# Kernel optimization log

Measured on AMD Instinct MI355X. Metric: run time of the kernel, lower is better.

Reference implementation:

```python
import jax, jax.numpy as jnp
import numpy as np

B, N, C, H, K = 4, 8192, 512, 8, 256
D = C // H  # head_dim = 64
EPS = 1e-6


def setup_inputs() -> dict:
    key = jax.random.key(0)
    k1, k2, k3 = jax.random.split(key, 3)
    x = jax.random.normal(k1, (B, N, C), dtype=jnp.float32)
    # Dense kernel (Keras default glorot-ish scale approximated; exact init irrelevant for math check)
    w_qkvv = jax.random.normal(k2, (C, 4 * C), dtype=jnp.float32) * (1.0 / np.sqrt(C))
    # UniformSqrtDim: uniform(-1/sqrt(K), 1/sqrt(K)) over shape (N, K)
    lim = 1.0 / np.sqrt(K)
    spatial_proj = jax.random.uniform(k3, (N, K), minval=-lim, maxval=lim, dtype=jnp.float32)
    temp_ca = jnp.ones((H, 1, 1), dtype=jnp.float32)
    temp_sa = jnp.ones((H, 1, 1), dtype=jnp.float32)
    return {"x": x, "w_qkvv": w_qkvv, "spatial_proj": spatial_proj,
            "temp_ca": temp_ca, "temp_sa": temp_sa}


def _safe_normalize(t):
    # normalize along last axis with clamped squared-sum (matches safe_normalize)
    sq = jnp.sum(t * t, axis=-1, keepdims=True)
    sq = jnp.where(sq < EPS, EPS, sq)
    return t / jnp.sqrt(sq)


def reference(x, w_qkvv, spatial_proj, temp_ca, temp_sa):
    b, n, c = x.shape
    qkvv = x @ w_qkvv  # [B, N, 4C]
    qkvv = qkvv.reshape(b, n, 4, H, D).transpose(2, 0, 3, 1, 4)  # [4, B, H, N, D]
    q, k, v_ca, v_sa = qkvv[0], qkvv[1], qkvv[2], qkvv[3]
    # transpose to [B, H, D, N]; normalize along N (tokens)
    q_t = q.transpose(0, 1, 3, 2)
    k_t = k.transpose(0, 1, 3, 2)
    v_ca_t = v_ca.transpose(0, 1, 3, 2)
    v_sa_t = v_sa.transpose(0, 1, 3, 2)
    q_norm = _safe_normalize(q_t)  # [B, H, D, N]
    k_norm = _safe_normalize(k_t)

    # --- Channel attention: [B,H,D,D] over small head_dim ---
    attn_ca = jnp.einsum('bhdn,bhen->bhde', q_norm, k_norm) * temp_ca
    attn_ca = jax.nn.softmax(attn_ca, axis=-1)
    x_ca = jnp.einsum('bhde,bhen->bhdn', attn_ca, v_ca_t)  # [B,H,D,N]
    x_ca = x_ca.transpose(0, 3, 1, 2).reshape(b, n, c)  # [B,N,C]

    # --- Spatial attention with N->K token projection ---
    k_proj = jnp.einsum('bhdn,nk->bhdk', k_norm, spatial_proj)  # [B,H,D,K]
    v_proj = jnp.einsum('bhdn,nk->bhdk', v_sa_t, spatial_proj)  # [B,H,D,K]
    attn_sa = jnp.einsum('bhdn,bhdk->bhnk', q_norm, k_proj) * temp_sa  # [B,H,N,K]
    attn_sa = jax.nn.softmax(attn_sa, axis=-1)
    x_sa = jnp.einsum('bhnk,bhdk->bhnd', attn_sa, v_proj)  # [B,H,N,D]
    x_sa = x_sa.transpose(0, 2, 1, 3).reshape(b, n, c)

    return x_ca + x_sa
```

## Files before the change

### kernel.cpp

```cpp
#include <hip/hip_runtime.h>
#include <hip/hip_bf16.h>

#define BATCH 4
#define SEQ   8192
#define CH    512
#define NHEAD 8
#define HDIM  64
#define KTOK  256
#define FOURC 2048

typedef __attribute__((ext_vector_type(8))) short bf16x8;
typedef __attribute__((ext_vector_type(4))) float f32x4;

#define GLOAD_LDS16(g, l)                                                      \
  __builtin_amdgcn_global_load_lds(                                            \
      (const __attribute__((address_space(1))) void*)(g),                      \
      (__attribute__((address_space(3))) void*)(l), 16, 0, 0)

__device__ __forceinline__ ushort bf16bits(float f) {
  __hip_bfloat16 b = __float2bfloat16(f);
  return *reinterpret_cast<ushort*>(&b);
}
__device__ __forceinline__ uint packbf2(float lo, float hi) {
  return (uint)bf16bits(lo) | ((uint)bf16bits(hi) << 16);
}

__global__ __launch_bounds__(256) void k_wt(
    const float* __restrict__ W, __hip_bfloat16* __restrict__ Wt) {
  __shared__ float tile[32][33];
  const int bx = blockIdx.x * 32;
  const int by = blockIdx.y * 32;
  const int t = threadIdx.x;
  const int r = t >> 5, c = t & 31;
#pragma unroll
  for (int it = 0; it < 4; ++it)
    tile[r + it * 8][c] = W[(size_t)(by + r + it * 8) * FOURC + bx + c];
  __syncthreads();
#pragma unroll
  for (int it = 0; it < 4; ++it) {
    int n = r + it * 8;
    Wt[(size_t)(bx + n) * CH + by + c] = __float2bfloat16(tile[c][n]);
  }
}

__global__ __launch_bounds__(256) void k_pt(
    const float* __restrict__ P, __hip_bfloat16* __restrict__ Pt) {
  __shared__ float tile[32][33];
  const int n0 = blockIdx.x * 32, k0 = blockIdx.y * 32;
  const int t = threadIdx.x, r = t >> 5, c = t & 31;
#pragma unroll
  for (int i = 0; i < 4; ++i)
    tile[r + i * 8][c] = P[(size_t)(n0 + r + i * 8) * KTOK + k0 + c];
  __syncthreads();
#pragma unroll
  for (int i = 0; i < 4; ++i)
    Pt[(size_t)(k0 + r + i * 8) * SEQ + n0 + c] = __float2bfloat16(tile[c][r + i * 8]);
}

__global__ __launch_bounds__(256) void k_xbf(
    const float* __restrict__ X, __hip_bfloat16* __restrict__ Xb) {
  size_t i = ((size_t)blockIdx.x * 256 + threadIdx.x) * 8;
  float4 a = *reinterpret_cast<const float4*>(&X[i]);
  float4 b = *reinterpret_cast<const float4*>(&X[i + 4]);
  ushort tmp[8];
  tmp[0] = bf16bits(a.x); tmp[1] = bf16bits(a.y);
  tmp[2] = bf16bits(a.z); tmp[3] = bf16bits(a.w);
  tmp[4] = bf16bits(b.x); tmp[5] = bf16bits(b.y);
  tmp[6] = bf16bits(b.z); tmp[7] = bf16bits(b.w);
  *reinterpret_cast<uint4*>(&Xb[i]) = *reinterpret_cast<const uint4*>(tmp);
}

__global__ __launch_bounds__(256) void k_gemm_mfma(
    const __hip_bfloat16* __restrict__ Xb, const __hip_bfloat16* __restrict__ Wt,
    __hip_bfloat16* __restrict__ QKVV) {
  __shared__ __align__(16) __hip_bfloat16 As[128 * 32];
  __shared__ __align__(16) __hip_bfloat16 Bs[128 * 32];
  const int t = threadIdx.x;
  const int wid = t >> 6, lane = t & 63;
  const int bid = blockIdx.x;
  const int xcd = bid & 7;
  const int l = bid >> 3;
  const int bm = (xcd * 32 + (l >> 4)) * 128;
  const int bn = (l & 15) * 128;
  const int wr = wid >> 1, wc = wid & 1;
  const int lrow = lane & 15, lk = (lane >> 4) * 8;
  const int srow = lane >> 2;
  const int sk8 = (lane & 3) * 8;
  f32x4 acc[4][4] = {};
  for (int k0 = 0; k0 < CH; k0 += 32) {
#pragma unroll
    for (int i = 0; i < 2; ++i) {
      const int c = wid * 2 + i;
      GLOAD_LDS16(&Xb[(size_t)(bm + c * 16 + srow) * CH + k0 + sk8], &As[c * 512]);
      GLOAD_LDS16(&Wt[(size_t)(bn + c * 16 + srow) * CH + k0 + sk8], &Bs[c * 512]);
    }
    __syncthreads();
    bf16x8 af[4], bfr[4];
#pragma unroll
    for (int i = 0; i < 4; ++i)
      af[i] = *reinterpret_cast<const bf16x8*>(&As[(wr * 64 + i * 16 + lrow) * 32 + lk]);
#pragma unroll
    for (int j = 0; j < 4; ++j)
      bfr[j] = *reinterpret_cast<const bf16x8*>(&Bs[(wc * 64 + j * 16 + lrow) * 32 + lk]);
#pragma unroll
    for (int i = 0; i < 4; ++i)
#pragma unroll
      for (int j = 0; j < 4; ++j)
        acc[i][j] = __builtin_amdgcn_mfma_f32_16x16x32_bf16(af[i], bfr[j], acc[i][j], 0, 0, 0);
    __syncthreads();
  }
  const int l4 = (lane >> 4) * 4;
#pragma unroll
  for (int i = 0; i < 4; ++i)
#pragma unroll
    for (int j = 0; j < 4; ++j) {
      int col = bn + wc * 64 + j * 16 + lrow;
#pragma unroll
      for (int r = 0; r < 4; ++r) {
        int row = bm + wr * 64 + i * 16 + l4 + r;
        QKVV[(size_t)row * FOURC + col] = __float2bfloat16(acc[i][j][r]);
      }
    }
}

__global__ __launch_bounds__(256) void k_finalize(
    const float* __restrict__ sumsq, float* __restrict__ invq, float* __restrict__ invk) {
  int i = blockIdx.x * 256 + threadIdx.x;
  if (i < 2048) {
    invq[i] = rsqrtf(fmaxf(sumsq[i], 1e-6f));
    invk[i] = rsqrtf(fmaxf(sumsq[2048 + i], 1e-6f));
  }
}

__global__ __launch_bounds__(256) void k_gram_stats(
    const __hip_bfloat16* __restrict__ QKVV, float* __restrict__ G,
    float* __restrict__ sumsq) {
  __shared__ __hip_bfloat16 qT[64][40];
  __shared__ __hip_bfloat16 kT[64][40];
  __shared__ float red[32][64];
  const int bh = blockIdx.y, b = bh >> 3, h = bh & 7;
  const int nbase = blockIdx.x * 512;
  const int t = threadIdx.x, w = t >> 6, lane = t & 63;
  const int l15 = lane & 15, g = lane >> 4;
  const int srow = t >> 3, sdq = (t & 7) * 8;
  f32x4 accg[4] = {};
  float sqq[8] = {}, sqk[8] = {};
  for (int n0 = nbase; n0 < nbase + 512; n0 += 32) {
    size_t gb = (size_t)(b * SEQ + n0 + srow) * FOURC + h * HDIM + sdq;
    uint4 uq = *reinterpret_cast<const uint4*>(&QKVV[gb]);
    uint4 uk = *reinterpret_cast<const uint4*>(&QKVV[gb + CH]);
    const __hip_bfloat16* hq = reinterpret_cast<const __hip_bfloat16*>(&uq);
    const __hip_bfloat16* hk = reinterpret_cast<const __hip_bfloat16*>(&uk);
#pragma unroll
    for (int j = 0; j < 8; ++j) {
      float fq = __bfloat162float(hq[j]);
      float fk = __bfloat162float(hk[j]);
      sqq[j] = fmaf(fq, fq, sqq[j]);
      sqk[j] = fmaf(fk, fk, sqk[j]);
      qT[sdq + j][srow] = hq[j];
      kT[sdq + j][srow] = hk[j];
    }
    __syncthreads();
    bf16x8 A[4];
#pragma unroll
    for (int dt = 0; dt < 4; ++dt)
      A[dt] = *reinterpret_cast<const bf16x8*>(&qT[dt * 16 + l15][g * 8]);
    bf16x8 B = *reinterpret_cast<const bf16x8*>(&kT[w * 16 + l15][g * 8]);
#pragma unroll
    for (int dt = 0; dt < 4; ++dt)
      accg[dt] = __builtin_amdgcn_mfma_f32_16x16x32_bf16(A[dt], B, accg[dt], 0, 0, 0);
    __syncthreads();
  }
#pragma unroll
  for (int j = 0; j < 8; ++j) red[srow][sdq + j] = sqq[j];
  __syncthreads();
  if (t < 64) {
    float tot = 0.f;
#pragma unroll
    for (int r = 0; r < 32; ++r) tot += red[r][t];
    atomicAdd(&sumsq[bh * 64 + t], tot);
  }
  __syncthreads();
#pragma unroll
  for (int j = 0; j < 8; ++j) red[srow][sdq + j] = sqk[j];
  __syncthreads();
  if (t < 64) {
    float tot = 0.f;
#pragma unroll
    for (int r = 0; r < 32; ++r) tot += red[r][t];
    atomicAdd(&sumsq[2048 + bh * 64 + t], tot);
  }
  float* gp = G + (size_t)bh * 4096;
#pragma unroll
  for (int dt = 0; dt < 4; ++dt)
#pragma unroll
    for (int r = 0; r < 4; ++r)
      atomicAdd(&gp[(dt * 16 + g * 4 + r) * 64 + w * 16 + l15], accg[dt][r]);
}

__global__ __launch_bounds__(64) void k_ca_softmax(
    float* __restrict__ G, const float* __restrict__ invq,
    const float* __restrict__ invk, const float* __restrict__ tca) {
  const int bh = blockIdx.x, h = bh & 7;
  const int d = threadIdx.x;
  float* row = G + (size_t)bh * 4096 + d * 64;
  const float s0 = invq[bh * 64 + d] * tca[h];
  float vals[64];
  float m = -3.0e38f;
#pragma unroll
  for (int e = 0; e < 64; ++e) {
    float v = row[e] * s0 * invk[bh * 64 + e];
    vals[e] = v;
    m = fmaxf(m, v);
  }
  float s = 0.f;
#pragma unroll
  for (int e = 0; e < 64; ++e) { vals[e] = __expf(vals[e] - m); s += vals[e]; }
  float r = 1.0f / s;
#pragma unroll
  for (int e = 0; e < 64; ++e) row[e] = vals[e] * r;
}

__global__ __launch_bounds__(256) void k_proj_mfma(
    const __hip_bfloat16* __restrict__ QKVV,
    const __hip_bfloat16* __restrict__ Pt,
    float* __restrict__ raw) {
  __shared__ __hip_bfloat16 cT[2][64][40];
  __shared__ __hip_bfloat16 pT[256][40];
  const int bh = blockIdx.y, b = bh >> 3, h = bh & 7;
  const int nbase = blockIdx.x * 1024;
  const int t = threadIdx.x, w = t >> 6, lane = t & 63;
  const int l15 = lane & 15, g = lane >> 4;
  const int comp = w >> 1, kh = w & 1;
  const int srow = t >> 3, sdq = (t & 7) * 8;
  f32x4 acc[4][8] = {};
  for (int n0 = nbase; n0 < nbase + 1024; n0 += 32) {
#pragma unroll
    for (int cc = 0; cc < 2; ++cc) {
      const int coff = cc ? 3 * CH : CH;
      uint4 u = *reinterpret_cast<const uint4*>(
          &QKVV[(size_t)(b * SEQ + n0 + srow) * FOURC + coff + h * HDIM + sdq]);
      const __hip_bfloat16* hp = reinterpret_cast<const __hip_bfloat16*>(&u);
#pragma unroll
      for (int j = 0; j < 8; ++j) cT[cc][sdq + j][srow] = hp[j];
    }
#pragma unroll
    for (int ps = 0; ps < 4; ++ps) {
      int k = ps * 64 + (t >> 2);
      int poff = (t & 3) * 8;
      *reinterpret_cast<uint4*>(&pT[k][poff]) =
          *reinterpret_cast<const uint4*>(&Pt[(size_t)k * SEQ + n0 + poff]);
    }
    __syncthreads();
    bf16x8 A[4], B[8];
#pragma unroll
    for (int dt = 0; dt < 4; ++dt)
      A[dt] = *reinterpret_cast<const bf16x8*>(&cT[comp][dt * 16 + l15][g * 8]);
#pragma unroll
    for (int kt = 0; kt < 8; ++kt)
      B[kt] = *reinterpret_cast<const bf16x8*>(&pT[(kh * 8 + kt) * 16 + l15][g * 8]);
#pragma unroll
    for (int dt = 0; dt < 4; ++dt)
#pragma unroll
      for (int kt = 0; kt < 8; ++kt)
        acc[dt][kt] = __builtin_amdgcn_mfma_f32_16x16x32_bf16(A[dt], B[kt], acc[dt][kt], 0, 0, 0);
    __syncthreads();
  }
  float* rp = raw + ((size_t)bh * 2 + comp) * (64 * 256);
#pragma unroll
  for (int dt = 0; dt < 4; ++dt)
#pragma unroll
    for (int kt = 0; kt < 8; ++kt)
#pragma unroll
      for (int r = 0; r < 4; ++r)
        atomicAdd(&rp[(dt * 16 + g * 4 + r) * 256 + (kh * 8 + kt) * 16 + l15],
                  acc[dt][kt][r]);
}

__global__ __launch_bounds__(256) void k_projfin(
    const float* __restrict__ raw, const float* __restrict__ invq,
    const float* __restrict__ invk, const float* __restrict__ tsa,
    __hip_bfloat16* __restrict__ kpT, __hip_bfloat16* __restrict__ vpT) {
  const int bh = blockIdx.x, h = bh & 7;
  const int t = threadIdx.x;
  __shared__ float tile[64][65];
  const float ts = tsa[h];
  const float* r0 = raw + (size_t)bh * 2 * 16384;
  for (int kc = 0; kc < 4; ++kc) {
    for (int i = t; i < 4096; i += 256) {
      int d = i >> 6, kk = i & 63;
      tile[d][kk] = r0[d * 256 + kc * 64 + kk];
    }
    __syncthreads();
    for (int i = t; i < 4096; i += 256) {
      int kk = i >> 6, d = i & 63;
      float sc = invq[bh * 64 + d] * invk[bh * 64 + d] * ts;
      kpT[(size_t)bh * 16384 + (kc * 64 + kk) * 64 + d] = __float2bfloat16(tile[d][kk] * sc);
    }
    __syncthreads();
  }
  const float* r1 = r0 + 16384;
  for (int i = t; i < 16384; i += 256)
    vpT[(size_t)bh * 16384 + i] = __float2bfloat16(r1[i]);
}

__global__ __launch_bounds__(256) void k_xout(
    const __hip_bfloat16* __restrict__ QKVV,
    const float* __restrict__ G,
    const __hip_bfloat16* __restrict__ kpT,
    const __hip_bfloat16* __restrict__ vpT,
    float* __restrict__ out) {
  __shared__ __hip_bfloat16 vs[64][264];
  __shared__ __hip_bfloat16 ps[4][16][264];
  __shared__ __hip_bfloat16 gs[64][72];
  const int bh = blockIdx.y, b = bh >> 3, h = bh & 7;
  const int nblk = blockIdx.x * 512;
  const int t = threadIdx.x, w = t >> 6, lane = t & 63;
  const int l15 = lane & 15, g = lane >> 4;
  for (int i = t; i < 2048; i += 256) {
    int d = i >> 5, k8 = (i & 31) * 8;
    *reinterpret_cast<uint4*>(&vs[d][k8]) =
        *reinterpret_cast<const uint4*>(&vpT[((size_t)bh * 64 + d) * 256 + k8]);
  }
  for (int i = t; i < 4096; i += 256)
    gs[i >> 6][i & 63] = __float2bfloat16(G[(size_t)bh * 4096 + i]);
  bf16x8 kA[2][16];
#pragma unroll
  for (int s = 0; s < 2; ++s)
#pragma unroll
    for (int f = 0; f < 16; ++f)
      kA[s][f] = *reinterpret_cast<const bf16x8*>(
          &kpT[((size_t)bh * 256 + f * 16 + l15) * 64 + s * 32 + g * 8]);
  __syncthreads();
  const __hip_bfloat16* qbase = QKVV + (size_t)b * SEQ * FOURC + h * HDIM;
  const __hip_bfloat16* vbase = qbase + 2 * CH;
  for (int c = w; c < 32; c += 4) {
    const int n0 = nblk + c * 16;
    bf16x8 qf[2], vf[2];
#pragma unroll
    for (int s = 0; s < 2; ++s) {
      qf[s] = *reinterpret_cast<const bf16x8*>(
          &qbase[(size_t)(n0 + l15) * FOURC + s * 32 + g * 8]);
      vf[s] = *reinterpret_cast<const bf16x8*>(
          &vbase[(size_t)(n0 + l15) * FOURC + s * 32 + g * 8]);
    }
    f32x4 o[4] = {};
#pragma unroll
    for (int dt = 0; dt < 4; ++dt) {
      bf16x8 g0 = *reinterpret_cast<const bf16x8*>(&gs[dt * 16 + l15][g * 8]);
      bf16x8 g1 = *reinterpret_cast<const bf16x8*>(&gs[dt * 16 + l15][32 + g * 8]);
      o[dt] = __builtin_amdgcn_mfma_f32_16x16x32_bf16(vf[0], g0, o[dt], 0, 0, 0);
      o[dt] = __builtin_amdgcn_mfma_f32_16x16x32_bf16(vf[1], g1, o[dt], 0, 0, 0);
    }
    f32x4 acc[16] = {};
#pragma unroll
    for (int f = 0; f < 16; ++f) {
      acc[f] = __builtin_amdgcn_mfma_f32_16x16x32_bf16(kA[0][f], qf[0], acc[f], 0, 0, 0);
      acc[f] = __builtin_amdgcn_mfma_f32_16x16x32_bf16(kA[1][f], qf[1], acc[f], 0, 0, 0);
    }
    float m = -3.0e38f;
#pragma unroll
    for (int f = 0; f < 16; ++f)
#pragma unroll
      for (int r = 0; r < 4; ++r) m = fmaxf(m, acc[f][r]);
    m = fmaxf(m, __shfl_xor(m, 16));
    m = fmaxf(m, __shfl_xor(m, 32));
    float sum = 0.f;
#pragma unroll
    for (int f = 0; f < 16; ++f)
#pragma unroll
      for (int r = 0; r < 4; ++r) {
        float e = __expf(acc[f][r] - m);
        acc[f][r] = e; sum += e;
      }
    sum += __shfl_xor(sum, 16);
    sum += __shfl_xor(sum, 32);
    const float rinv = 1.0f / sum;
#pragma unroll
    for (int f = 0; f < 16; ++f) {
      uint2 pw;
      pw.x = packbf2(acc[f][0] * rinv, acc[f][1] * rinv);
      pw.y = packbf2(acc[f][2] * rinv, acc[f][3] * rinv);
      *reinterpret_cast<uint2*>(&ps[w][l15][f * 16 + g * 4]) = pw;
    }
    __builtin_amdgcn_wave_barrier();
#pragma unroll
    for (int s = 0; s < 8; ++s) {
      bf16x8 pa = *reinterpret_cast<const bf16x8*>(&ps[w][l15][s * 32 + g * 8]);
#pragma unroll
      for (int dt = 0; dt < 4; ++dt) {
        bf16x8 vb = *reinterpret_cast<const bf16x8*>(&vs[dt * 16 + l15][s * 32 + g * 8]);
        o[dt] = __builtin_amdgcn_mfma_f32_16x16x32_bf16(pa, vb, o[dt], 0, 0, 0);
      }
    }
#pragma unroll
    for (int dt = 0; dt < 4; ++dt)
#pragma unroll
      for (int r = 0; r < 4; ++r) {
        size_t oo = ((size_t)(b * SEQ + n0 + g * 4 + r)) * CH + h * HDIM + dt * 16 + l15;
        out[oo] = o[dt][r];
      }
    __builtin_amdgcn_wave_barrier();
  }
}

extern "C" void kernel_launch(void* const* d_in, const int* in_sizes, int n_in,
                              void* d_out, int out_size, void* d_ws, size_t ws_size,
                              hipStream_t stream) {
  const float* x   = (const float*)d_in[0];
  const float* w   = (const float*)d_in[1];
  const float* sp  = (const float*)d_in[2];
  const float* tca = (const float*)d_in[3];
  const float* tsa = (const float*)d_in[4];
  float* out = (float*)d_out;
  char* ws = (char*)d_ws;

  __hip_bfloat16* qkvv = (__hip_bfloat16*)ws;
  __hip_bfloat16* wt   = (__hip_bfloat16*)(ws + 134217728);
  __hip_bfloat16* pt   = (__hip_bfloat16*)(ws + 136314880);
  __hip_bfloat16* xb   = (__hip_bfloat16*)(ws + 140509184);
  __hip_bfloat16* kpT  = (__hip_bfloat16*)(ws + 174063616);
  __hip_bfloat16* vpT  = (__hip_bfloat16*)(ws + 175112192);
  float* invq  = (float*)(ws + 176160768);
  float* invk  = (float*)(ws + 176168960);
  float* G     = (float*)(ws + 176177152);
  float* sumsq = (float*)(ws + 176701440);
  float* raw   = (float*)(ws + 176717824);

  hipMemsetAsync(G, 0, 524288 + 16384 + 4194304, stream);

  hipLaunchKernelGGL(k_wt, dim3(64, 16), dim3(256), 0, stream, w, wt);
  hipLaunchKernelGGL(k_pt, dim3(256, 8), dim3(256), 0, stream, sp, pt);
  hipLaunchKernelGGL(k_xbf, dim3(8192), dim3(256), 0, stream, x, xb);
  hipLaunchKernelGGL(k_gemm_mfma, dim3(4096), dim3(256), 0, stream, xb, wt, qkvv);
  hipLaunchKernelGGL(k_gram_stats, dim3(16, 32), dim3(256), 0, stream, qkvv, G, sumsq);
  hipLaunchKernelGGL(k_proj_mfma, dim3(8, 32), dim3(256), 0, stream, qkvv, pt, raw);
  hipLaunchKernelGGL(k_finalize, dim3(8), dim3(256), 0, stream, sumsq, invq, invk);
  hipLaunchKernelGGL(k_ca_softmax, dim3(32), dim3(64), 0, stream, G, invq, invk, tca);
  hipLaunchKernelGGL(k_projfin, dim3(32), dim3(256), 0, stream, raw, invq, invk, tsa, kpT, vpT);
  hipLaunchKernelGGL(k_xout, dim3(16, 32), dim3(256), 0, stream, qkvv, G, kpT, vpT, out);
}
```

Baseline: 310.4 us.

## Fuse Gram/stats with spatial projection and swizzle GEMM LDS layout

Merges the Q/K Gram-and-sum-of-squares kernel with the K/V spatial projection kernel, so the K tile is loaded from QKVV once per block and both reductions run in one pass with one fewer launch. The merged kernel uses the projection kernel's 1024-token chunks, which halves the block count of the Gram pass and raises register and LDS use per block. Separately, the GEMM's LDS write and read column indices are XOR-swizzled to reduce bank conflicts on the fragment loads. The swizzle must match exactly between the global_load_lds writes and the MFMA fragment reads, or results will be wrong.

```diff
diff --git a/kernel.cpp b/kernel.cpp
--- a/kernel.cpp
+++ b/kernel.cpp
@@ -83,9 +83,10 @@
   const int bm = (xcd * 32 + (l >> 4)) * 128;
   const int bn = (l & 15) * 128;
   const int wr = wid >> 1, wc = wid & 1;
-  const int lrow = lane & 15, lk = (lane >> 4) * 8;
+  const int lrow = lane & 15;
+  const int lk = (((lane >> 4) ^ ((lrow >> 1) & 3))) * 8;
   const int srow = lane >> 2;
-  const int sk8 = (lane & 3) * 8;
+  const int sk8 = (((lane & 3) ^ ((lane >> 3) & 3))) * 8;
   f32x4 acc[4][4] = {};
   for (int k0 = 0; k0 < CH; k0 += 32) {
 #pragma unroll
@@ -132,25 +133,32 @@
   }
 }
 
-__global__ __launch_bounds__(256) void k_gram_stats(
-    const __hip_bfloat16* __restrict__ QKVV, float* __restrict__ G,
-    float* __restrict__ sumsq) {
+__global__ __launch_bounds__(256) void k_qkstats(
+    const __hip_bfloat16* __restrict__ QKVV,
+    const __hip_bfloat16* __restrict__ Pt,
+    float* __restrict__ G, float* __restrict__ sumsq, float* __restrict__ raw) {
   __shared__ __hip_bfloat16 qT[64][40];
   __shared__ __hip_bfloat16 kT[64][40];
+  __shared__ __hip_bfloat16 vT[64][40];
+  __shared__ __hip_bfloat16 pT[256][40];
   __shared__ float red[32][64];
   const int bh = blockIdx.y, b = bh >> 3, h = bh & 7;
-  const int nbase = blockIdx.x * 512;
+  const int nbase = blockIdx.x * 1024;
   const int t = threadIdx.x, w = t >> 6, lane = t & 63;
   const int l15 = lane & 15, g = lane >> 4;
+  const int comp = w >> 1, kh = w & 1;
   const int srow = t >> 3, sdq = (t & 7) * 8;
+  f32x4 acc[4][8] = {};
   f32x4 accg[4] = {};
   float sqq[8] = {}, sqk[8] = {};
-  for (int n0 = nbase; n0 < nbase + 512; n0 += 32) {
+  for (int n0 = nbase; n0 < nbase + 1024; n0 += 32) {
     size_t gb = (size_t)(b * SEQ + n0 + srow) * FOURC + h * HDIM + sdq;
     uint4 uq = *reinterpret_cast<const uint4*>(&QKVV[gb]);
     uint4 uk = *reinterpret_cast<const uint4*>(&QKVV[gb + CH]);
+    uint4 uv = *reinterpret_cast<const uint4*>(&QKVV[gb + 3 * CH]);
     const __hip_bfloat16* hq = reinterpret_cast<const __hip_bfloat16*>(&uq);
     const __hip_bfloat16* hk = reinterpret_cast<const __hip_bfloat16*>(&uk);
+    const __hip_bfloat16* hv = reinterpret_cast<const __hip_bfloat16*>(&uv);
 #pragma unroll
     for (int j = 0; j < 8; ++j) {
       float fq = __bfloat162float(hq[j]);
@@ -159,16 +167,41 @@
       sqk[j] = fmaf(fk, fk, sqk[j]);
       qT[sdq + j][srow] = hq[j];
       kT[sdq + j][srow] = hk[j];
-    }
-    __syncthreads();
-    bf16x8 A[4];
-#pragma unroll
-    for (int dt = 0; dt < 4; ++dt)
-      A[dt] = *reinterpret_cast<const bf16x8*>(&qT[dt * 16 + l15][g * 8]);
-    bf16x8 B = *reinterpret_cast<const bf16x8*>(&kT[w * 16 + l15][g * 8]);
-#pragma unroll
-    for (int dt = 0; dt < 4; ++dt)
-      accg[dt] = __builtin_amdgcn_mfma_f32_16x16x32_bf16(A[dt], B, accg[dt], 0, 0, 0);
+      vT[sdq + j][srow] = hv[j];
+    }
+#pragma unroll
+    for (int ps = 0; ps < 4; ++ps) {
+      int k = ps * 64 + (t >> 2);
+      int poff = (t & 3) * 8;
+      *reinterpret_cast<uint4*>(&pT[k][poff]) =
+          *reinterpret_cast<const uint4*>(&Pt[(size_t)k * SEQ + n0 + poff]);
+    }
+    __syncthreads();
+    {
+      bf16x8 Aq[4];
+#pragma unroll
+      for (int dt = 0; dt < 4; ++dt)
+        Aq[dt] = *reinterpret_cast<const bf16x8*>(&qT[dt * 16 + l15][g * 8]);
+      bf16x8 Bk = *reinterpret_cast<const bf16x8*>(&kT[w * 16 + l15][g * 8]);
+#pragma unroll
+      for (int dt = 0; dt < 4; ++dt)
+        accg[dt] = __builtin_amdgcn_mfma_f32_16x16x32_bf16(Aq[dt], Bk, accg[dt], 0, 0, 0);
+    }
+    {
+      bf16x8 A[4], B[8];
+#pragma unroll
+      for (int dt = 0; dt < 4; ++dt)
+        A[dt] = comp ? *reinterpret_cast<const bf16x8*>(&vT[dt * 16 + l15][g * 8])
+                     : *reinterpret_cast<const bf16x8*>(&kT[dt * 16 + l15][g * 8]);
+#pragma unroll
+      for (int kt = 0; kt < 8; ++kt)
+        B[kt] = *reinterpret_cast<const bf16x8*>(&pT[(kh * 8 + kt) * 16 + l15][g * 8]);
+#pragma unroll
+      for (int dt = 0; dt < 4; ++dt)
+#pragma unroll
+        for (int kt = 0; kt < 8; ++kt)
+          acc[dt][kt] = __builtin_amdgcn_mfma_f32_16x16x32_bf16(A[dt], B[kt], acc[dt][kt], 0, 0, 0);
+    }
     __syncthreads();
   }
 #pragma unroll
@@ -196,6 +229,15 @@
 #pragma unroll
     for (int r = 0; r < 4; ++r)
       atomicAdd(&gp[(dt * 16 + g * 4 + r) * 64 + w * 16 + l15], accg[dt][r]);
+  float* rp = raw + ((size_t)bh * 2 + comp) * (64 * 256);
+#pragma unroll
+  for (int dt = 0; dt < 4; ++dt)
+#pragma unroll
+    for (int kt = 0; kt < 8; ++kt)
+#pragma unroll
+      for (int r = 0; r < 4; ++r)
+        atomicAdd(&rp[(dt * 16 + g * 4 + r) * 256 + (kh * 8 + kt) * 16 + l15],
+                  acc[dt][kt][r]);
 }
 
 __global__ __launch_bounds__(64) void k_ca_softmax(
@@ -219,62 +261,6 @@
   float r = 1.0f / s;
 #pragma unroll
   for (int e = 0; e < 64; ++e) row[e] = vals[e] * r;
-}
-
-__global__ __launch_bounds__(256) void k_proj_mfma(
-    const __hip_bfloat16* __restrict__ QKVV,
-    const __hip_bfloat16* __restrict__ Pt,
-    float* __restrict__ raw) {
-  __shared__ __hip_bfloat16 cT[2][64][40];
-  __shared__ __hip_bfloat16 pT[256][40];
-  const int bh = blockIdx.y, b = bh >> 3, h = bh & 7;
-  const int nbase = blockIdx.x * 1024;
-  const int t = threadIdx.x, w = t >> 6, lane = t & 63;
-  const int l15 = lane & 15, g = lane >> 4;
-  const int comp = w >> 1, kh = w & 1;
-  const int srow = t >> 3, sdq = (t & 7) * 8;
-  f32x4 acc[4][8] = {};
-  for (int n0 = nbase; n0 < nbase + 1024; n0 += 32) {
-#pragma unroll
-    for (int cc = 0; cc < 2; ++cc) {
-      const int coff = cc ? 3 * CH : CH;
-      uint4 u = *reinterpret_cast<const uint4*>(
-          &QKVV[(size_t)(b * SEQ + n0 + srow) * FOURC + coff + h * HDIM + sdq]);
-      const __hip_bfloat16* hp = reinterpret_cast<const __hip_bfloat16*>(&u);
-#pragma unroll
-      for (int j = 0; j < 8; ++j) cT[cc][sdq + j][srow] = hp[j];
-    }
-#pragma unroll
-    for (int ps = 0; ps < 4; ++ps) {
-      int k = ps * 64 + (t >> 2);
-      int poff = (t & 3) * 8;
-      *reinterpret_cast<uint4*>(&pT[k][poff]) =
-          *reinterpret_cast<const uint4*>(&Pt[(size_t)k * SEQ + n0 + poff]);
-    }
-    __syncthreads();
-    bf16x8 A[4], B[8];
-#pragma unroll
-    for (int dt = 0; dt < 4; ++dt)
-      A[dt] = *reinterpret_cast<const bf16x8*>(&cT[comp][dt * 16 + l15][g * 8]);
-#pragma unroll
-    for (int kt = 0; kt < 8; ++kt)
-      B[kt] = *reinterpret_cast<const bf16x8*>(&pT[(kh * 8 + kt) * 16 + l15][g * 8]);
-#pragma unroll
-    for (int dt = 0; dt < 4; ++dt)
-#pragma unroll
-      for (int kt = 0; kt < 8; ++kt)
-        acc[dt][kt] = __builtin_amdgcn_mfma_f32_16x16x32_bf16(A[dt], B[kt], acc[dt][kt], 0, 0, 0);
-    __syncthreads();
-  }
-  float* rp = raw + ((size_t)bh * 2 + comp) * (64 * 256);
-#pragma unroll
-  for (int dt = 0; dt < 4; ++dt)
-#pragma unroll
-    for (int kt = 0; kt < 8; ++kt)
-#pragma unroll
-      for (int r = 0; r < 4; ++r)
-        atomicAdd(&rp[(dt * 16 + g * 4 + r) * 256 + (kh * 8 + kt) * 16 + l15],
-                  acc[dt][kt][r]);
 }
 
 __global__ __launch_bounds__(256) void k_projfin(
@@ -433,8 +419,7 @@
   hipLaunchKernelGGL(k_pt, dim3(256, 8), dim3(256), 0, stream, sp, pt);
   hipLaunchKernelGGL(k_xbf, dim3(8192), dim3(256), 0, stream, x, xb);
   hipLaunchKernelGGL(k_gemm_mfma, dim3(4096), dim3(256), 0, stream, xb, wt, qkvv);
-  hipLaunchKernelGGL(k_gram_stats, dim3(16, 32), dim3(256), 0, stream, qkvv, G, sumsq);
-  hipLaunchKernelGGL(k_proj_mfma, dim3(8, 32), dim3(256), 0, stream, qkvv, pt, raw);
+  hipLaunchKernelGGL(k_qkstats, dim3(8, 32), dim3(256), 0, stream, qkvv, pt, G, sumsq, raw);
   hipLaunchKernelGGL(k_finalize, dim3(8), dim3(256), 0, stream, sumsq, invq, invk);
   hipLaunchKernelGGL(k_ca_softmax, dim3(32), dim3(64), 0, stream, G, invq, invk, tca);
   hipLaunchKernelGGL(k_projfin, dim3(32), dim3(256), 0, stream, raw, invq, invk, tsa, kpT, vpT);
```

Result: faster. 290.5 us (-6.4%).
